# Kernel tuning notes

Hardware: AMD Instinct MI355X
Metric: run time of the kernel (lower is better)

The kernel has to match this reference:

```python
import jax, jax.numpy as jnp
import numpy as np

B, C, Q, D = 64, 512, 64, 256  # D = 2 * hidden_size; similarity weight has 3*D = 768 entries


def _length_mask(key, batch, seqlen):
    # realistic padding masks: each row has a random valid prefix length in [seqlen//2, seqlen]
    lens = jax.random.randint(key, (batch,), seqlen // 2, seqlen + 1)
    return (jnp.arange(seqlen)[None, :] < lens[:, None]).astype(jnp.int32)


def setup_inputs() -> dict:
    key = jax.random.key(0)
    k1, k2, k3, k4, k5 = jax.random.split(key, 5)
    context = jax.random.normal(k1, (B, C, D), dtype=jnp.float32)
    question = jax.random.normal(k2, (B, Q, D), dtype=jnp.float32)
    context_mask = _length_mask(k3, B, C)
    question_mask = _length_mask(k4, B, Q)
    w = jax.random.normal(k5, (3 * D,), dtype=jnp.float32) * (1.0 / np.sqrt(3 * D))
    return {"context": context, "question": question,
            "context_mask": context_mask, "question_mask": question_mask, "w": w}


def reference(context, question, context_mask, question_mask, w):
    d = context.shape[-1]
    # Linear([c, q, c*q]) with no bias decomposes exactly into three terms.
    w_c, w_q, w_m = w[:d], w[d:2 * d], w[2 * d:]
    sim = ((context @ w_c)[:, :, None]                      # [B, C, 1]
           + (question @ w_q)[:, None, :]                   # [B, 1, Q]
           + jnp.einsum('bcd,bqd->bcq', context * w_m, question))  # [B, C, Q]
    neg = jnp.finfo(sim.dtype).min
    # context-to-query attention (mask question positions)
    sim_q = jnp.where(question_mask[:, None, :] != 0, sim, neg)
    a = jax.nn.softmax(sim_q, axis=2)                        # [B, C, Q]
    c2q = jnp.einsum('bcq,bqd->bcd', a, question)            # [B, C, D]
    # query-to-context attention (max over Q, mask context positions)
    sim_max = jnp.max(sim, axis=2)                           # [B, C]
    sim_max = jnp.where(context_mask != 0, sim_max, neg)
    b = jax.nn.softmax(sim_max, axis=1)                      # [B, C]
    q2c = jnp.einsum('bc,bcd->bd', b, context)[:, None, :]   # [B, 1, D]
    q2c = jnp.broadcast_to(q2c, context.shape)               # [B, C, D]
    g = jnp.concatenate([context, c2q, context * c2q, context * q2c], axis=-1)
    return g
```

## Files before the change

### kernel.cpp

```cpp
#include <hip/hip_runtime.h>
#include <hip/hip_bf16.h>
#include <float.h>

#define B_ 64
#define C_ 512
#define Q_ 64
#define D_ 256

typedef _Float16 f16x8 __attribute__((ext_vector_type(8)));
typedef float f32x4 __attribute__((ext_vector_type(4)));

union U4H8 { uint4 u; f16x8 h; };
union UH2 { _Float16 h[2]; uint32_t u; };

__device__ __forceinline__ uint32_t packh2(float a, float b) {
  UH2 v; v.h[0] = (_Float16)a; v.h[1] = (_Float16)b; return v.u;
}

__device__ __forceinline__ float wred_sum(float v) {
#pragma unroll
  for (int off = 32; off > 0; off >>= 1) v += __shfl_xor(v, off, 64);
  return v;
}
__device__ __forceinline__ float wred_max(float v) {
#pragma unroll
  for (int off = 32; off > 0; off >>= 1) v = fmaxf(v, __shfl_xor(v, off, 64));
  return v;
}

__global__ __launch_bounds__(256) void k_rowdot(const float* __restrict__ src,
                                                const float* __restrict__ wgt,
                                                float* __restrict__ out, int nrows) {
  int wv = threadIdx.x >> 6, ln = threadIdx.x & 63;
  int row = blockIdx.x * 4 + wv;
  if (row >= nrows) return;
  float4 s4 = *(const float4*)(src + (size_t)row * D_ + 4 * ln);
  float4 w4 = *(const float4*)(wgt + 4 * ln);
  float p = s4.x * w4.x + s4.y * w4.y + s4.z * w4.z + s4.w * w4.w;
  p = wred_sum(p);
  if (ln == 0) out[row] = p;
}

__global__ __launch_bounds__(256, 2) void k_main(
    const float* __restrict__ ctx, const float* __restrict__ qst,
    const int* __restrict__ qmask, const float* __restrict__ w,
    const float* __restrict__ qwq_g, float* __restrict__ g,
    float* __restrict__ simmax_g) {
  __shared__ __align__(16) ushort qraw[Q_ * D_];
  __shared__ __align__(16) ushort qT[D_ * Q_];
  __shared__ __align__(16) ushort pbuf[4][16 * Q_];
  __shared__ float qwq_l[Q_];
  __shared__ int   qml_l[Q_];

  const int bid = blockIdx.x;
  const int b = bid & 63;
  const int c0 = (bid >> 6) * 64;
  const int t = threadIdx.x;
  const int wv = t >> 6, ln = t & 63;
  const int lc = ln & 15;
  const int lg = ln >> 4;
  const int c0w = c0 + wv * 16;

  f16x8 bfrag[8];
  float cwc_p = 0.f;
  const float* crow = ctx + ((size_t)b * C_ + c0w + lc) * D_;
  float* grow0 = g + ((size_t)b * C_ + c0w + lc) * (4 * D_);
#pragma unroll
  for (int kk = 0; kk < 8; ++kk) {
    int kb = kk * 32 + lg * 8;
    float4 cv0 = *(const float4*)(crow + kb);
    float4 cv1 = *(const float4*)(crow + kb + 4);
    float4 wc0 = *(const float4*)(w + kb);
    float4 wc1 = *(const float4*)(w + kb + 4);
    float4 wm0 = *(const float4*)(w + 2 * D_ + kb);
    float4 wm1 = *(const float4*)(w + 2 * D_ + kb + 4);
    cwc_p += cv0.x * wc0.x + cv0.y * wc0.y + cv0.z * wc0.z + cv0.w * wc0.w
           + cv1.x * wc1.x + cv1.y * wc1.y + cv1.z * wc1.z + cv1.w * wc1.w;
    bfrag[kk][0] = (_Float16)(cv0.x * wm0.x);
    bfrag[kk][1] = (_Float16)(cv0.y * wm0.y);
    bfrag[kk][2] = (_Float16)(cv0.z * wm0.z);
    bfrag[kk][3] = (_Float16)(cv0.w * wm0.w);
    bfrag[kk][4] = (_Float16)(cv1.x * wm1.x);
    bfrag[kk][5] = (_Float16)(cv1.y * wm1.y);
    bfrag[kk][6] = (_Float16)(cv1.z * wm1.z);
    bfrag[kk][7] = (_Float16)(cv1.w * wm1.w);
    *(float4*)(grow0 + kb) = cv0;
    *(float4*)(grow0 + kb + 4) = cv1;
  }
  float cwc = cwc_p;
  cwc += __shfl_xor(cwc, 16, 64);
  cwc += __shfl_xor(cwc, 32, 64);

  const float* qb = qst + (size_t)b * Q_ * D_;
#pragma unroll 4
  for (int it = 0; it < 32; ++it) {
    int idx = it * 256 + t;
    int q = idx >> 7, jp = idx & 127;
    float2 v = *(const float2*)(qb + q * D_ + 2 * jp);
    int ch = jp >> 2;
    int phys = (ch & ~7) | ((ch & 7) ^ (q & 7));
    *(uint32_t*)((char*)qraw + q * 512 + phys * 16 + (jp & 3) * 4) = packh2(v.x, v.y);
  }
#pragma unroll 4
  for (int it = 0; it < 32; ++it) {
    int q = t & 63;
    int jp = (t >> 6) + 4 * it;
    float2 v = *(const float2*)(qb + q * D_ + 2 * jp);
    int d0 = 2 * jp, d1 = d0 + 1;
    UH2 h0; h0.h[0] = (_Float16)v.x;
    UH2 h1; h1.h[0] = (_Float16)v.y;
    *(ushort*)((char*)qT + d0 * 128 + (((q >> 3) ^ (d0 & 7)) << 4) + (q & 7) * 2) = (ushort)(h0.u & 0xffff);
    *(ushort*)((char*)qT + d1 * 128 + (((q >> 3) ^ (d1 & 7)) << 4) + (q & 7) * 2) = (ushort)(h1.u & 0xffff);
  }
  if (t < Q_) { qwq_l[t] = qwq_g[b * Q_ + t]; qml_l[t] = qmask[b * Q_ + t]; }
  __syncthreads();

  f32x4 sacc[4];
#pragma unroll
  for (int tq = 0; tq < 4; ++tq) sacc[tq] = f32x4{0.f, 0.f, 0.f, 0.f};
#pragma unroll
  for (int tq = 0; tq < 4; ++tq) {
    int q = 16 * tq + lc;
#pragma unroll
    for (int kk = 0; kk < 8; ++kk) {
      int ch = lg + 4 * kk;
      int phys = (ch & ~7) | ((ch & 7) ^ (q & 7));
      U4H8 a; a.u = *(const uint4*)((const char*)qraw + q * 512 + phys * 16);
      sacc[tq] = __builtin_amdgcn_mfma_f32_16x16x32_f16(a.h, bfrag[kk], sacc[tq], 0, 0, 0);
    }
  }

  float vals[4][4];
  float rmax = -FLT_MAX;
#pragma unroll
  for (int tq = 0; tq < 4; ++tq) {
    float4 qw4 = *(const float4*)(qwq_l + 16 * tq + 4 * lg);
#pragma unroll
    for (int r = 0; r < 4; ++r) {
      float qv = (r == 0) ? qw4.x : (r == 1) ? qw4.y : (r == 2) ? qw4.z : qw4.w;
      vals[tq][r] = sacc[tq][r] + cwc + qv;
      rmax = fmaxf(rmax, vals[tq][r]);
    }
  }
  rmax = fmaxf(rmax, __shfl_xor(rmax, 16, 64));
  rmax = fmaxf(rmax, __shfl_xor(rmax, 32, 64));
  if (ln < 16) simmax_g[b * C_ + c0w + lc] = rmax;

  float mmax = -FLT_MAX;
#pragma unroll
  for (int tq = 0; tq < 4; ++tq) {
    int4 qm4 = *(const int4*)(qml_l + 16 * tq + 4 * lg);
#pragma unroll
    for (int r = 0; r < 4; ++r) {
      int m = (r == 0) ? qm4.x : (r == 1) ? qm4.y : (r == 2) ? qm4.z : qm4.w;
      vals[tq][r] = m ? vals[tq][r] : -FLT_MAX;
      mmax = fmaxf(mmax, vals[tq][r]);
    }
  }
  mmax = fmaxf(mmax, __shfl_xor(mmax, 16, 64));
  mmax = fmaxf(mmax, __shfl_xor(mmax, 32, 64));
  float esum = 0.f;
#pragma unroll
  for (int tq = 0; tq < 4; ++tq)
#pragma unroll
    for (int r = 0; r < 4; ++r) {
      vals[tq][r] = __expf(vals[tq][r] - mmax);
      esum += vals[tq][r];
    }
  esum += __shfl_xor(esum, 16, 64);
  esum += __shfl_xor(esum, 32, 64);
  float inv = 1.f / esum;
#pragma unroll
  for (int tq = 0; tq < 4; ++tq) {
    uint32_t p01 = packh2(vals[tq][0] * inv, vals[tq][1] * inv);
    uint32_t p23 = packh2(vals[tq][2] * inv, vals[tq][3] * inv);
    int qb4 = 16 * tq + 4 * lg;
    int phys = ((qb4 >> 3) ^ (lc & 7));
    char* dst = (char*)pbuf[wv] + lc * 128 + phys * 16 + (qb4 & 7) * 2;
    *(uint2*)dst = uint2{p01, p23};
  }

  f16x8 pfragB[2];
#pragma unroll
  for (int ks = 0; ks < 2; ++ks) {
    int phys = (lg + 4 * ks) ^ (lc & 7);
    U4H8 a; a.u = *(const uint4*)((const char*)pbuf[wv] + lc * 128 + phys * 16);
    pfragB[ks] = a.h;
  }
  const float* crow2 = ctx + ((size_t)b * C_ + c0w + lc) * D_;
  float* grow = g + ((size_t)b * C_ + c0w + lc) * (4 * D_);
#pragma unroll 4
  for (int dt = 0; dt < 16; ++dt) {
    f32x4 acc = f32x4{0.f, 0.f, 0.f, 0.f};
#pragma unroll
    for (int ks = 0; ks < 2; ++ks) {
      int d = dt * 16 + lc;
      int phys = (lg + 4 * ks) ^ (d & 7);
      U4H8 aq; aq.u = *(const uint4*)((const char*)qT + d * 128 + phys * 16);
      acc = __builtin_amdgcn_mfma_f32_16x16x32_f16(aq.h, pfragB[ks], acc, 0, 0, 0);
    }
    int dcol = dt * 16 + 4 * lg;
    float4 cvv = *(const float4*)(crow2 + dcol);
    float4 c2qv{acc[0], acc[1], acc[2], acc[3]};
    *(float4*)(grow + D_ + dcol) = c2qv;
    float4 p2{cvv.x * c2qv.x, cvv.y * c2qv.y, cvv.z * c2qv.z, cvv.w * c2qv.w};
    *(float4*)(grow + 2 * D_ + dcol) = p2;
  }
}

__global__ __launch_bounds__(256) void k_q2c_bs(const float* __restrict__ ctx,
                                                const float* __restrict__ simmax,
                                                const int* __restrict__ cmask,
                                                float* __restrict__ part) {
  int b = blockIdx.x, ch = blockIdx.y, t = threadIdx.x;
  int wv = t >> 6, ln = t & 63;
  __shared__ float bls[C_];
  __shared__ float sred[4];
  __shared__ float ssum[4];
  float v0 = simmax[b * C_ + t], v1 = simmax[b * C_ + 256 + t];
  if (!cmask[b * C_ + t]) v0 = -FLT_MAX;
  if (!cmask[b * C_ + 256 + t]) v1 = -FLT_MAX;
  float mx = wred_max(fmaxf(v0, v1));
  if (ln == 0) sred[wv] = mx;
  __syncthreads();
  float bm = fmaxf(fmaxf(sred[0], sred[1]), fmaxf(sred[2], sred[3]));
  float e0 = __expf(v0 - bm), e1 = __expf(v1 - bm);
  float ps = wred_sum(e0 + e1);
  if (ln == 0) ssum[wv] = ps;
  __syncthreads();
  float bs = ssum[0] + ssum[1] + ssum[2] + ssum[3];
  float invbs = 1.f / bs;
  bls[t] = e0 * invbs;
  bls[256 + t] = e1 * invbs;
  __syncthreads();
  float acc = 0.f;
  int cbeg = ch * 64;
#pragma unroll 4
  for (int c = cbeg; c < cbeg + 64; ++c)
    acc += bls[c] * ctx[((size_t)b * C_ + c) * D_ + t];
  part[((size_t)b * 8 + ch) * D_ + t] = acc;
}

__global__ __launch_bounds__(256) void k_q2c_sum(const float* __restrict__ part,
                                                 float* __restrict__ q2c) {
  int b = blockIdx.x, t = threadIdx.x;
  float s = 0.f;
#pragma unroll
  for (int ch = 0; ch < 8; ++ch) s += part[((size_t)b * 8 + ch) * D_ + t];
  q2c[b * D_ + t] = s;
}

__global__ __launch_bounds__(256) void k_g3(const float* __restrict__ ctx,
                                            const float* __restrict__ q2c,
                                            float* __restrict__ g) {
  size_t i = (size_t)blockIdx.x * 256 + threadIdx.x;
  int d4 = (int)(i & 63);
  size_t row = i >> 6;
  int b = (int)(row >> 9);
  float4 cv = *(const float4*)(ctx + row * D_ + 4 * d4);
  float4 qv = *(const float4*)(q2c + (size_t)b * D_ + 4 * d4);
  float4 o{cv.x * qv.x, cv.y * qv.y, cv.z * qv.z, cv.w * qv.w};
  *(float4*)(g + row * (4 * D_) + 3 * D_ + 4 * d4) = o;
}

extern "C" void kernel_launch(void* const* d_in, const int* in_sizes, int n_in,
                              void* d_out, int out_size, void* d_ws, size_t ws_size,
                              hipStream_t stream) {
  const float* ctx   = (const float*)d_in[0];
  const float* qst   = (const float*)d_in[1];
  const int*   cmask = (const int*)d_in[2];
  const int*   qmask = (const int*)d_in[3];
  const float* w     = (const float*)d_in[4];
  float* g  = (float*)d_out;
  float* ws = (float*)d_ws;

  float* qwq    = ws;
  float* simmax = ws + 4096;
  float* part   = ws + 36864;
  float* q2c    = ws + 167936;

  k_rowdot<<<dim3(B_ * Q_ / 4), 256, 0, stream>>>(qst, w + D_, qwq, B_ * Q_);
  k_main<<<dim3(512), 256, 0, stream>>>(ctx, qst, qmask, w, qwq, g, simmax);
  k_q2c_bs<<<dim3(B_, 8), 256, 0, stream>>>(ctx, simmax, cmask, part);
  k_q2c_sum<<<dim3(B_), 256, 0, stream>>>(part, q2c);
  k_g3<<<dim3(B_ * C_ * 64 / 256), 256, 0, stream>>>(ctx, q2c, g);
}
```

Measured before the change: 65.78 us.

## Split each 16-row tile across two waves in k_main with 512-thread blocks

Doubles k_main's block size to 512 threads so each 16-context-row tile is handled by a pair of waves. Each wave of the pair computes half the query columns of the similarity, the softmax reductions are combined through shared memory, and each wave produces half the D columns of c2q. The aim is more waves in flight and shorter per-wave latency for the same grid. The cost is extra __syncthreads and shared-memory exchanges, plus duplicated context loads and bfrag construction in both waves of a pair.

```diff
diff --git a/kernel.cpp b/kernel.cpp
--- a/kernel.cpp
+++ b/kernel.cpp
@@ -41,7 +41,7 @@
   if (ln == 0) out[row] = p;
 }
 
-__global__ __launch_bounds__(256, 2) void k_main(
+__global__ __launch_bounds__(512, 4) void k_main(
     const float* __restrict__ ctx, const float* __restrict__ qst,
     const int* __restrict__ qmask, const float* __restrict__ w,
     const float* __restrict__ qwq_g, float* __restrict__ g,
@@ -51,15 +51,20 @@
   __shared__ __align__(16) ushort pbuf[4][16 * Q_];
   __shared__ float qwq_l[Q_];
   __shared__ int   qml_l[Q_];
+  __shared__ float sred_raw[8][16];
+  __shared__ float sred_msk[8][16];
+  __shared__ float ssum[8][16];
 
   const int bid = blockIdx.x;
   const int b = bid & 63;
   const int c0 = (bid >> 6) * 64;
   const int t = threadIdx.x;
   const int wv = t >> 6, ln = t & 63;
+  const int p = wv >> 1;
+  const int h = wv & 1;
   const int lc = ln & 15;
   const int lg = ln >> 4;
-  const int c0w = c0 + wv * 16;
+  const int c0w = c0 + p * 16;
 
   f16x8 bfrag[8];
   float cwc_p = 0.f;
@@ -84,8 +89,10 @@
     bfrag[kk][5] = (_Float16)(cv1.y * wm1.y);
     bfrag[kk][6] = (_Float16)(cv1.z * wm1.z);
     bfrag[kk][7] = (_Float16)(cv1.w * wm1.w);
-    *(float4*)(grow0 + kb) = cv0;
-    *(float4*)(grow0 + kb + 4) = cv1;
+    if (h == 0) {
+      *(float4*)(grow0 + kb) = cv0;
+      *(float4*)(grow0 + kb + 4) = cv1;
+    }
   }
   float cwc = cwc_p;
   cwc += __shfl_xor(cwc, 16, 64);
@@ -93,8 +100,8 @@
 
   const float* qb = qst + (size_t)b * Q_ * D_;
 #pragma unroll 4
-  for (int it = 0; it < 32; ++it) {
-    int idx = it * 256 + t;
+  for (int it = 0; it < 16; ++it) {
+    int idx = it * 512 + t;
     int q = idx >> 7, jp = idx & 127;
     float2 v = *(const float2*)(qb + q * D_ + 2 * jp);
     int ch = jp >> 2;
@@ -102,9 +109,9 @@
     *(uint32_t*)((char*)qraw + q * 512 + phys * 16 + (jp & 3) * 4) = packh2(v.x, v.y);
   }
 #pragma unroll 4
-  for (int it = 0; it < 32; ++it) {
+  for (int it = 0; it < 16; ++it) {
     int q = t & 63;
-    int jp = (t >> 6) + 4 * it;
+    int jp = (t >> 6) + 8 * it;
     float2 v = *(const float2*)(qb + q * D_ + 2 * jp);
     int d0 = 2 * jp, d1 = d0 + 1;
     UH2 h0; h0.h[0] = (_Float16)v.x;
@@ -115,82 +122,85 @@
   if (t < Q_) { qwq_l[t] = qwq_g[b * Q_ + t]; qml_l[t] = qmask[b * Q_ + t]; }
   __syncthreads();
 
-  f32x4 sacc[4];
-#pragma unroll
-  for (int tq = 0; tq < 4; ++tq) sacc[tq] = f32x4{0.f, 0.f, 0.f, 0.f};
-#pragma unroll
-  for (int tq = 0; tq < 4; ++tq) {
-    int q = 16 * tq + lc;
+  f32x4 sacc[2];
+#pragma unroll
+  for (int i = 0; i < 2; ++i) sacc[i] = f32x4{0.f, 0.f, 0.f, 0.f};
+#pragma unroll
+  for (int i = 0; i < 2; ++i) {
+    int q = 16 * (2 * h + i) + lc;
 #pragma unroll
     for (int kk = 0; kk < 8; ++kk) {
       int ch = lg + 4 * kk;
       int phys = (ch & ~7) | ((ch & 7) ^ (q & 7));
       U4H8 a; a.u = *(const uint4*)((const char*)qraw + q * 512 + phys * 16);
-      sacc[tq] = __builtin_amdgcn_mfma_f32_16x16x32_f16(a.h, bfrag[kk], sacc[tq], 0, 0, 0);
-    }
-  }
-
-  float vals[4][4];
-  float rmax = -FLT_MAX;
-#pragma unroll
-  for (int tq = 0; tq < 4; ++tq) {
-    float4 qw4 = *(const float4*)(qwq_l + 16 * tq + 4 * lg);
+      sacc[i] = __builtin_amdgcn_mfma_f32_16x16x32_f16(a.h, bfrag[kk], sacc[i], 0, 0, 0);
+    }
+  }
+
+  float vals[2][4];
+  float rmax_h = -FLT_MAX, mmax_h = -FLT_MAX;
+#pragma unroll
+  for (int i = 0; i < 2; ++i) {
+    int qb4 = 16 * (2 * h + i) + 4 * lg;
+    float4 qw4 = *(const float4*)(qwq_l + qb4);
+    int4   qm4 = *(const int4*)(qml_l + qb4);
 #pragma unroll
     for (int r = 0; r < 4; ++r) {
       float qv = (r == 0) ? qw4.x : (r == 1) ? qw4.y : (r == 2) ? qw4.z : qw4.w;
-      vals[tq][r] = sacc[tq][r] + cwc + qv;
-      rmax = fmaxf(rmax, vals[tq][r]);
-    }
-  }
-  rmax = fmaxf(rmax, __shfl_xor(rmax, 16, 64));
-  rmax = fmaxf(rmax, __shfl_xor(rmax, 32, 64));
-  if (ln < 16) simmax_g[b * C_ + c0w + lc] = rmax;
-
-  float mmax = -FLT_MAX;
-#pragma unroll
-  for (int tq = 0; tq < 4; ++tq) {
-    int4 qm4 = *(const int4*)(qml_l + 16 * tq + 4 * lg);
+      int   m  = (r == 0) ? qm4.x : (r == 1) ? qm4.y : (r == 2) ? qm4.z : qm4.w;
+      float s = sacc[i][r] + cwc + qv;
+      rmax_h = fmaxf(rmax_h, s);
+      vals[i][r] = m ? s : -FLT_MAX;
+      mmax_h = fmaxf(mmax_h, vals[i][r]);
+    }
+  }
+  rmax_h = fmaxf(rmax_h, __shfl_xor(rmax_h, 16, 64));
+  rmax_h = fmaxf(rmax_h, __shfl_xor(rmax_h, 32, 64));
+  mmax_h = fmaxf(mmax_h, __shfl_xor(mmax_h, 16, 64));
+  mmax_h = fmaxf(mmax_h, __shfl_xor(mmax_h, 32, 64));
+  if (ln < 16) { sred_raw[wv][lc] = rmax_h; sred_msk[wv][lc] = mmax_h; }
+  __syncthreads();
+  float rmax = fmaxf(rmax_h, sred_raw[wv ^ 1][lc]);
+  float mmax = fmaxf(mmax_h, sred_msk[wv ^ 1][lc]);
+  if (h == 0 && ln < 16) simmax_g[b * C_ + c0w + lc] = rmax;
+
+  float esum_h = 0.f;
+#pragma unroll
+  for (int i = 0; i < 2; ++i)
 #pragma unroll
     for (int r = 0; r < 4; ++r) {
-      int m = (r == 0) ? qm4.x : (r == 1) ? qm4.y : (r == 2) ? qm4.z : qm4.w;
-      vals[tq][r] = m ? vals[tq][r] : -FLT_MAX;
-      mmax = fmaxf(mmax, vals[tq][r]);
-    }
-  }
-  mmax = fmaxf(mmax, __shfl_xor(mmax, 16, 64));
-  mmax = fmaxf(mmax, __shfl_xor(mmax, 32, 64));
-  float esum = 0.f;
-#pragma unroll
-  for (int tq = 0; tq < 4; ++tq)
-#pragma unroll
-    for (int r = 0; r < 4; ++r) {
-      vals[tq][r] = __expf(vals[tq][r] - mmax);
-      esum += vals[tq][r];
-    }
-  esum += __shfl_xor(esum, 16, 64);
-  esum += __shfl_xor(esum, 32, 64);
+      vals[i][r] = __expf(vals[i][r] - mmax);
+      esum_h += vals[i][r];
+    }
+  esum_h += __shfl_xor(esum_h, 16, 64);
+  esum_h += __shfl_xor(esum_h, 32, 64);
+  if (ln < 16) ssum[wv][lc] = esum_h;
+  __syncthreads();
+  float esum = esum_h + ssum[wv ^ 1][lc];
   float inv = 1.f / esum;
 #pragma unroll
-  for (int tq = 0; tq < 4; ++tq) {
-    uint32_t p01 = packh2(vals[tq][0] * inv, vals[tq][1] * inv);
-    uint32_t p23 = packh2(vals[tq][2] * inv, vals[tq][3] * inv);
-    int qb4 = 16 * tq + 4 * lg;
+  for (int i = 0; i < 2; ++i) {
+    uint32_t p01 = packh2(vals[i][0] * inv, vals[i][1] * inv);
+    uint32_t p23 = packh2(vals[i][2] * inv, vals[i][3] * inv);
+    int qb4 = 16 * (2 * h + i) + 4 * lg;
     int phys = ((qb4 >> 3) ^ (lc & 7));
-    char* dst = (char*)pbuf[wv] + lc * 128 + phys * 16 + (qb4 & 7) * 2;
+    char* dst = (char*)pbuf[p] + lc * 128 + phys * 16 + (qb4 & 7) * 2;
     *(uint2*)dst = uint2{p01, p23};
   }
+  __syncthreads();
 
   f16x8 pfragB[2];
 #pragma unroll
   for (int ks = 0; ks < 2; ++ks) {
     int phys = (lg + 4 * ks) ^ (lc & 7);
-    U4H8 a; a.u = *(const uint4*)((const char*)pbuf[wv] + lc * 128 + phys * 16);
+    U4H8 a; a.u = *(const uint4*)((const char*)pbuf[p] + lc * 128 + phys * 16);
     pfragB[ks] = a.h;
   }
   const float* crow2 = ctx + ((size_t)b * C_ + c0w + lc) * D_;
   float* grow = g + ((size_t)b * C_ + c0w + lc) * (4 * D_);
 #pragma unroll 4
-  for (int dt = 0; dt < 16; ++dt) {
+  for (int j = 0; j < 8; ++j) {
+    int dt = 8 * h + j;
     f32x4 acc = f32x4{0.f, 0.f, 0.f, 0.f};
 #pragma unroll
     for (int ks = 0; ks < 2; ++ks) {
@@ -280,7 +290,7 @@
   float* q2c    = ws + 167936;
 
   k_rowdot<<<dim3(B_ * Q_ / 4), 256, 0, stream>>>(qst, w + D_, qwq, B_ * Q_);
-  k_main<<<dim3(512), 256, 0, stream>>>(ctx, qst, qmask, w, qwq, g, simmax);
+  k_main<<<dim3(512), 512, 0, stream>>>(ctx, qst, qmask, w, qwq, g, simmax);
   k_q2c_bs<<<dim3(B_, 8), 256, 0, stream>>>(ctx, simmax, cmask, part);
   k_q2c_sum<<<dim3(B_), 256, 0, stream>>>(part, q2c);
   k_g3<<<dim3(B_ * C_ * 64 / 256), 256, 0, stream>>>(ctx, q2c, g);
```

Result: slower. 99.76 us (+51.7%).
